# Kernel tuning notes

Hardware: AMD Instinct MI355X
Metric: run time of the kernel (lower is better)

Reference implementation:

```python
import jax, jax.numpy as jnp
import numpy as np

B, DIM, NUM_HEADS = 16384, 2048, 4
SD = DIM // 2            # single_dim = 1024
HD = SD // NUM_HEADS     # head_dim = 256
LH = SD // 4             # lambda-net hidden = 256
SCALE = HD ** -0.5


def setup_inputs() -> dict:
    key = jax.random.key(0)
    ks = jax.random.split(key, 20)
    w = lambda k, shape: jax.random.normal(k, shape, dtype=jnp.float32) * 0.02
    inp = {
        "x": jax.random.normal(ks[0], (B, DIM), dtype=jnp.float32),
        # Linear weights stored (in, out); y = x @ W + b (equivalent to torch Linear)
        "WQ1_w": w(ks[1], (SD, SD)), "WQ1_b": jnp.zeros((SD,), jnp.float32),
        "WK1_w": w(ks[2], (SD, SD)), "WK1_b": jnp.zeros((SD,), jnp.float32),
        "WQ2_w": w(ks[3], (SD, SD)), "WQ2_b": jnp.zeros((SD,), jnp.float32),
        "WK2_w": w(ks[4], (SD, SD)), "WK2_b": jnp.zeros((SD,), jnp.float32),
        "WV_w": w(ks[5], (SD, SD)), "WV_b": jnp.zeros((SD,), jnp.float32),
        "WO_w": w(ks[6], (SD, SD)), "WO_b": jnp.zeros((SD,), jnp.float32),
        "L1_w": w(ks[7], (DIM, LH)), "L1_b": jnp.zeros((LH,), jnp.float32),
        "L2_w": w(ks[8], (LH, 1)), "L2_b": jnp.zeros((1,), jnp.float32),
    }
    return inp


def _heads(t, W, b):
    # tokens [B,2,SD] -> [B,H,2,HD]
    y = t @ W + b
    return y.reshape(B, 2, NUM_HEADS, HD).transpose(0, 2, 1, 3)


def reference(x, WQ1_w, WQ1_b, WK1_w, WK1_b, WQ2_w, WQ2_b, WK2_w, WK2_b,
              WV_w, WV_b, WO_w, WO_b, L1_w, L1_b, L2_w, L2_b):
    tokens = x.reshape(B, 2, SD)
    # gating lambda in (0,1): MLP(x) -> [B,1,1,1]
    lam = jax.nn.sigmoid(jax.nn.relu(x @ L1_w + L1_b) @ L2_w + L2_b)
    lam = lam.reshape(B, 1, 1, 1)

    Q1 = _heads(tokens, WQ1_w, WQ1_b)
    K1 = _heads(tokens, WK1_w, WK1_b)
    Q2 = _heads(tokens, WQ2_w, WQ2_b)
    K2 = _heads(tokens, WK2_w, WK2_b)
    V = _heads(tokens, WV_w, WV_b)

    attn1 = jax.nn.softmax(jnp.einsum("bhqd,bhkd->bhqk", Q1, K1) * SCALE, axis=-1)
    attn2 = jax.nn.softmax(jnp.einsum("bhqd,bhkd->bhqk", Q2, K2) * SCALE, axis=-1)
    diff_attn = jax.nn.relu(attn1 - lam * attn2)  # dropout = identity (eval)

    out = jnp.einsum("bhqk,bhkd->bhqd", diff_attn, V)  # [B,H,2,HD]
    out = out.transpose(0, 2, 1, 3).reshape(B, 2, SD)
    out = (out @ WO_w + WO_b) + tokens
    return out.reshape(B, SD * 2)
```

## Files before the change

### kernel.cpp

```cpp
#include <hip/hip_runtime.h>
#include <stdint.h>


#define BATCH  16384
#define ATT_SCALE 0.0625f

typedef __attribute__((ext_vector_type(8)))  short   s16x8;
typedef __attribute__((ext_vector_type(4)))  float   f32x4;
typedef __attribute__((ext_vector_type(2)))  float   f32x2;
typedef __attribute__((ext_vector_type(8)))  int     i32x8;
typedef __attribute__((ext_vector_type(8)))  unsigned short u16x8;
typedef __attribute__((ext_vector_type(4)))  unsigned short u16x4;

__device__ __forceinline__ unsigned short f2bf(float f) {
  unsigned u = __float_as_uint(f);
  u += 0x7FFFu + ((u >> 16) & 1u);
  return (unsigned short)(u >> 16);
}
__device__ __forceinline__ float bf2f(unsigned short s) {
  return __uint_as_float((unsigned)s << 16);
}

__device__ __forceinline__ unsigned char f2e4m3(float f) {
  unsigned u = __float_as_uint(f);
  unsigned s = (u >> 24) & 0x80u;
  float a = fabsf(f);
  if (a >= 448.f) return (unsigned char)(s | 0x7E);
  if (a < 0.0009765625f) return (unsigned char)s;
  int e = (int)((u >> 23) & 0xFF) - 127;
  if (e < -6) {
    int q = (int)rintf(a * 512.f);
    if (q >= 8) return (unsigned char)(s | 0x08);
    return (unsigned char)(s | q);
  }
  unsigned mant = u & 0x7FFFFFu;
  unsigned mr = mant + 0x7FFFFu + ((mant >> 20) & 1u);
  e += (int)(mr >> 23);
  mant = (mr >> 20) & 7u;
  if (e > 8) return (unsigned char)(s | 0x7E);
  return (unsigned char)(s | ((e + 7) << 3) | mant);
}
__device__ __forceinline__ float e4m3f(unsigned v) {
  unsigned e = (v >> 3) & 15u, m = v & 7u;
  float mag = (e == 0) ? (float)m * 0.001953125f
                       : __uint_as_float(((e + 120u) << 23) | (m << 20));
  return (v & 0x80u) ? -mag : mag;
}

__device__ __forceinline__ unsigned char cvt1_fp8(float v) {
#if __has_builtin(__builtin_amdgcn_cvt_pk_fp8_f32)
  return (unsigned char)(__builtin_amdgcn_cvt_pk_fp8_f32(v, v, 0, false) & 0xff);
#else
  return f2e4m3(v);
#endif
}

__device__ __forceinline__ void dec8(uint2 p, float* o) {
#if __has_builtin(__builtin_amdgcn_cvt_pk_f32_fp8)
  f32x2 a = __builtin_amdgcn_cvt_pk_f32_fp8((int)p.x, false);
  f32x2 b = __builtin_amdgcn_cvt_pk_f32_fp8((int)p.x, true);
  f32x2 c = __builtin_amdgcn_cvt_pk_f32_fp8((int)p.y, false);
  f32x2 d = __builtin_amdgcn_cvt_pk_f32_fp8((int)p.y, true);
  o[0] = a[0]; o[1] = a[1]; o[2] = b[0]; o[3] = b[1];
  o[4] = c[0]; o[5] = c[1]; o[6] = d[0]; o[7] = d[1];
#else
#pragma unroll
  for (int j = 0; j < 4; ++j) o[j]     = e4m3f((p.x >> (8 * j)) & 255u);
#pragma unroll
  for (int j = 0; j < 4; ++j) o[4 + j] = e4m3f((p.y >> (8 * j)) & 255u);
#endif
}

__device__ __forceinline__ void async16(const void* g, void* l) {
  __builtin_amdgcn_global_load_lds((__attribute__((address_space(1))) void*)g,
                                   (__attribute__((address_space(3))) void*)l,
                                   16, 0, 0);
}

__global__ __launch_bounds__(512, 2)
void gemm_mx(const unsigned char* __restrict__ A,
             const unsigned char* __restrict__ Bt,
             const float* __restrict__ bias,
             unsigned char* __restrict__ Cout,
             unsigned char* __restrict__ Vout,
             int NN,
             const unsigned short* __restrict__ xbf,
             const unsigned short* __restrict__ lamBt,
             const float* __restrict__ lamL1b,
             const float* __restrict__ lamL2w,
             float* __restrict__ lamp)
{
  __shared__ __align__(16) char lds[131072];
  const int tid  = threadIdx.x;
  const int lane = tid & 63, w = tid >> 6;
  const int wm = w >> 2, wn = w & 3;
  const int li = lane & 15, lc = lane >> 4;

  if (blockIdx.x < 128) {
    const int bm_l = blockIdx.x * 128;
    const int t = tid;
    const size_t aSrc  = (size_t)(bm_l + (t >> 2)) * 2048 + (t & 3) * 8;
    const size_t b0Src = (size_t)(t >> 2) * 2048 + (t & 3) * 8;
    const size_t b1Src = (size_t)(128 + (t >> 2)) * 2048 + (t & 3) * 8;

    f32x4 acc[4][4];
#pragma unroll
    for (int i = 0; i < 4; ++i)
#pragma unroll
      for (int j = 0; j < 4; ++j) acc[i][j] = (f32x4)0.f;

    for (int k0 = 0; k0 < 2048; k0 += 32) {
      async16(xbf   + aSrc  + k0, lds + w * 1024);
      async16(lamBt + b0Src + k0, lds + 8192 + w * 1024);
      async16(lamBt + b1Src + k0, lds + 16384 + w * 1024);
      __syncthreads();
      s16x8 aR[4], bR[4];
#pragma unroll
      for (int m = 0; m < 4; ++m)
        aR[m] = *(const s16x8*)(lds + ((w >> 2) * 64 + m * 16 + li) * 64 + lc * 16);
#pragma unroll
      for (int n = 0; n < 4; ++n)
        bR[n] = *(const s16x8*)(lds + 8192 + ((w & 3) * 64 + n * 16 + li) * 64 + lc * 16);
#pragma unroll
      for (int m = 0; m < 4; ++m)
#pragma unroll
        for (int n = 0; n < 4; ++n)
          acc[m][n] = __builtin_amdgcn_mfma_f32_16x16x32_bf16(aR[m], bR[n], acc[m][n], 0, 0, 0);
      __syncthreads();
    }

    float l2v[4], bvv[4];
#pragma unroll
    for (int n = 0; n < 4; ++n) {
      const int col = (w & 3) * 64 + n * 16 + li;
      l2v[n] = lamL2w[col];
      bvv[n] = lamL1b[col];
    }
#pragma unroll
    for (int m = 0; m < 4; ++m)
#pragma unroll
      for (int j = 0; j < 4; ++j) {
        float part = 0.f;
#pragma unroll
        for (int n = 0; n < 4; ++n)
          part += fmaxf(acc[m][n][j] + bvv[n], 0.f) * l2v[n];
        part += __shfl_xor(part, 1, 64);
        part += __shfl_xor(part, 2, 64);
        part += __shfl_xor(part, 4, 64);
        part += __shfl_xor(part, 8, 64);
        if ((lane & 15) == 0)
          atomicAdd(lamp + bm_l + (w >> 2) * 64 + m * 16 + lc * 4 + j, part);
      }
    return;
  }

  const int bid = blockIdx.x - 128;
  const int nwg = 2560;
  const int swz = (bid & 7) * (nwg >> 3) + (bid >> 3);
  const int bm = (swz / NN) * 256;
  const int bn = (swz % NN) * 256;

  const int grow   = lane >> 3;
  const int gchunk = ((lane & 7) ^ grow) * 16;
  size_t aSrc[4], bSrc[4];
  int dstKB[4];
#pragma unroll
  for (int i = 0; i < 4; ++i) {
    const int rr = (i * 8 + w) * 8 + grow;
    aSrc[i] = (size_t)(bm + rr) * 1024 + gchunk;
    bSrc[i] = (size_t)(bn + rr) * 1024 + gchunk;
    dstKB[i] = (i * 8 + w) * 1024;
  }

  const int x7   = li & 7;
  const int off0 = ((2 * lc)     ^ x7) * 16;
  const int off1 = ((2 * lc + 1) ^ x7) * 16;
  const int aRow = (wm * 128 + li) * 128;
  const int bRow = 32768 + (wn * 64 + li) * 128;

  f32x4 acc[8][4];
#pragma unroll
  for (int m = 0; m < 8; ++m)
#pragma unroll
    for (int n = 0; n < 4; ++n) acc[m][n] = (f32x4)0.f;

#pragma unroll
  for (int i = 0; i < 4; ++i) {
    async16(A  + aSrc[i], lds + dstKB[i]);
    async16(Bt + bSrc[i], lds + 32768 + dstKB[i]);
  }
#pragma unroll
  for (int i = 0; i < 4; ++i) {
    async16(A  + aSrc[i] + 128, lds + 65536 + dstKB[i]);
    async16(Bt + bSrc[i] + 128, lds + 98304 + dstKB[i]);
  }
  asm volatile("s_waitcnt vmcnt(8)" ::: "memory");
  __builtin_amdgcn_s_barrier();

  for (int t = 0; t < 8; ++t) {
    char* buf = lds + (t & 1) * 65536;

    i32x8 bF[4];
#pragma unroll
    for (int nf = 0; nf < 4; ++nf) {
      const char* p = buf + bRow + nf * 2048;
      uint4* bp = (uint4*)&bF[nf];
      bp[0] = *(const uint4*)(p + off0);
      bp[1] = *(const uint4*)(p + off1);
    }
#pragma unroll
    for (int mh = 0; mh < 2; ++mh) {
      i32x8 aF[4];
#pragma unroll
      for (int mf = 0; mf < 4; ++mf) {
        const char* p = buf + aRow + (mh * 4 + mf) * 2048;
        uint4* ap = (uint4*)&aF[mf];
        ap[0] = *(const uint4*)(p + off0);
        ap[1] = *(const uint4*)(p + off1);
      }
      __builtin_amdgcn_s_setprio(1);
#pragma unroll
      for (int mf = 0; mf < 4; ++mf)
#pragma unroll
        for (int nf = 0; nf < 4; ++nf)
          acc[mh * 4 + mf][nf] = __builtin_amdgcn_mfma_scale_f32_16x16x128_f8f6f4(
              aF[mf], bF[nf], acc[mh * 4 + mf][nf],
              0, 0, 0, 0x7F7F7F7F, 0, 0x7F7F7F7F);
      __builtin_amdgcn_s_setprio(0);
    }
    __builtin_amdgcn_s_barrier();
    if (t + 2 < 8) {
      const size_t kt = (size_t)(t + 2) * 128;
#pragma unroll
      for (int i = 0; i < 4; ++i) {
        async16(A  + aSrc[i] + kt, buf + dstKB[i]);
        async16(Bt + bSrc[i] + kt, buf + 32768 + dstKB[i]);
      }
    }
    if (t < 6) { asm volatile("s_waitcnt vmcnt(8)" ::: "memory"); }
    else       { asm volatile("s_waitcnt vmcnt(0)" ::: "memory"); }
    __builtin_amdgcn_s_barrier();
  }

  float bv[4];
#pragma unroll
  for (int n = 0; n < 4; ++n) bv[n] = bias[bn + wn * 64 + n * 16 + li];

  if (bn < 4096) {
    unsigned char* wl0 = (unsigned char*)(lds + w * 12288);
#pragma unroll
    for (int mp = 0; mp < 4; ++mp) {
      unsigned char* wl = wl0 + (mp & 1) * 2560;
#pragma unroll
      for (int mi = 0; mi < 2; ++mi)
#pragma unroll
        for (int jj = 0; jj < 4; ++jj) {
          unsigned d = 0;
#pragma unroll
          for (int n = 0; n < 4; ++n) {
            float v = acc[mp * 2 + mi][n][jj] + bv[n];
            d |= (unsigned)cvt1_fp8(v) << (8 * n);
          }
          *(unsigned*)(wl + (mi * 16 + lc * 4 + jj) * 80 + li * 4) = d;
        }
      const size_t base = (size_t)((bm + wm * 128 + mp * 32) >> 5) * 131072
                        + (size_t)((bn >> 6) + wn) * 2048;
      uint4 v0 = *(const uint4*)(wl + (lane >> 2) * 80 + (lane & 3) * 16);
      *(uint4*)(Cout + base + lane * 16) = v0;
      uint4 v1 = *(const uint4*)(wl + (16 + (lane >> 2)) * 80 + (lane & 3) * 16);
      *(uint4*)(Cout + base + 1024 + lane * 16) = v1;
    }
  } else {
    unsigned char* wl0 = (unsigned char*)(lds + w * 12288);
    const int cb = bn - 4096;
#pragma unroll
    for (int mp = 0; mp < 4; ++mp) {
      unsigned char* wl = wl0 + (mp & 1) * 2560;
#pragma unroll
      for (int mi = 0; mi < 2; ++mi)
#pragma unroll
        for (int n = 0; n < 4; ++n)
#pragma unroll
          for (int jj = 0; jj < 4; ++jj) {
            float v = acc[mp * 2 + mi][n][jj] + bv[n];
            wl[(mi * 16 + lc * 4 + jj) * 72 + n * 16 + li] = cvt1_fp8(v);
          }
#pragma unroll
      for (int i = 0; i < 4; ++i) {
        const int rr = i * 8 + (lane >> 3);
        uint2 vv = *(const uint2*)(wl + rr * 72 + (lane & 7) * 8);
        const size_t gi = (size_t)(bm + wm * 128 + mp * 32 + rr) * 1024
                        + cb + wn * 64 + (lane & 7) * 8;
        *(uint2*)(Vout + gi) = vv;
      }
    }
  }
}

__global__ __launch_bounds__(512, 2)
void gemm_womx(const unsigned char* __restrict__ A,
               const unsigned char* __restrict__ Bt,
               const float* __restrict__ bias,
               float* __restrict__ Cout,
               const unsigned short* __restrict__ res)
{
  __shared__ __align__(16) char lds[131072];
  const int tid  = threadIdx.x;
  const int lane = tid & 63, w = tid >> 6;
  const int wm = w >> 2, wn = w & 3;
  const int li = lane & 15, lc = lane >> 4;

  const int swz = (blockIdx.x & 7) * 64 + (blockIdx.x >> 3);
  const int bm = (swz >> 2) * 256;
  const int bn = (swz & 3) * 256;

  const int grow   = lane >> 3;
  const int gchunk = ((lane & 7) ^ grow) * 16;
  size_t aSrc[4], bSrc[4];
  int dstKB[4];
#pragma unroll
  for (int i = 0; i < 4; ++i) {
    const int rr = (i * 8 + w) * 8 + grow;
    aSrc[i] = (size_t)(bm + rr) * 1024 + gchunk;
    bSrc[i] = (size_t)(bn + rr) * 1024 + gchunk;
    dstKB[i] = (i * 8 + w) * 1024;
  }

  const int x7   = li & 7;
  const int off0 = ((2 * lc)     ^ x7) * 16;
  const int off1 = ((2 * lc + 1) ^ x7) * 16;
  const int aRow = (wm * 128 + li) * 128;
  const int bRow = 32768 + (wn * 64 + li) * 128;

  f32x4 acc[8][4];
#pragma unroll
  for (int m = 0; m < 8; ++m)
#pragma unroll
    for (int n = 0; n < 4; ++n) acc[m][n] = (f32x4)0.f;

#pragma unroll
  for (int i = 0; i < 4; ++i) {
    async16(A  + aSrc[i], lds + dstKB[i]);
    async16(Bt + bSrc[i], lds + 32768 + dstKB[i]);
  }
#pragma unroll
  for (int i = 0; i < 4; ++i) {
    async16(A  + aSrc[i] + 128, lds + 65536 + dstKB[i]);
    async16(Bt + bSrc[i] + 128, lds + 98304 + dstKB[i]);
  }
  asm volatile("s_waitcnt vmcnt(8)" ::: "memory");
  __builtin_amdgcn_s_barrier();

  for (int t = 0; t < 8; ++t) {
    char* buf = lds + (t & 1) * 65536;

    i32x8 bF[4];
#pragma unroll
    for (int nf = 0; nf < 4; ++nf) {
      const char* p = buf + bRow + nf * 2048;
      uint4* bp = (uint4*)&bF[nf];
      bp[0] = *(const uint4*)(p + off0);
      bp[1] = *(const uint4*)(p + off1);
    }
#pragma unroll
    for (int mh = 0; mh < 2; ++mh) {
      i32x8 aF[4];
#pragma unroll
      for (int mf = 0; mf < 4; ++mf) {
        const char* p = buf + aRow + (mh * 4 + mf) * 2048;
        uint4* ap = (uint4*)&aF[mf];
        ap[0] = *(const uint4*)(p + off0);
        ap[1] = *(const uint4*)(p + off1);
      }
      __builtin_amdgcn_s_setprio(1);
#pragma unroll
      for (int mf = 0; mf < 4; ++mf)
#pragma unroll
        for (int nf = 0; nf < 4; ++nf)
          acc[mh * 4 + mf][nf] = __builtin_amdgcn_mfma_scale_f32_16x16x128_f8f6f4(
              aF[mf], bF[nf], acc[mh * 4 + mf][nf],
              0, 0, 0, 0x7F7F7F7F, 0, 0x7F7F7F7F);
      __builtin_amdgcn_s_setprio(0);
    }
    __builtin_amdgcn_s_barrier();
    if (t + 2 < 8) {
      const size_t kt = (size_t)(t + 2) * 128;
#pragma unroll
      for (int i = 0; i < 4; ++i) {
        async16(A  + aSrc[i] + kt, buf + dstKB[i]);
        async16(Bt + bSrc[i] + kt, buf + 32768 + dstKB[i]);
      }
    }
    if (t < 6) { asm volatile("s_waitcnt vmcnt(8)" ::: "memory"); }
    else       { asm volatile("s_waitcnt vmcnt(0)" ::: "memory"); }
    __builtin_amdgcn_s_barrier();
  }

  float bv[4];
#pragma unroll
  for (int n = 0; n < 4; ++n) bv[n] = bias[bn + wn * 64 + n * 16 + li];

  float* wl0 = (float*)(lds + w * 12288);
#pragma unroll
  for (int m = 0; m < 8; ++m) {
    float* wl = wl0 + (m & 1) * 1088;
#pragma unroll
    for (int n = 0; n < 4; ++n)
#pragma unroll
      for (int jj = 0; jj < 4; ++jj)
        wl[(lc * 4 + jj) * 68 + li + n * 16] = acc[m][n][jj] + bv[n];
#pragma unroll
    for (int i = 0; i < 4; ++i) {
      const int rr = i * 4 + lc;
      f32x4 vv = *(const f32x4*)(wl + rr * 68 + li * 4);
      const size_t gi = (size_t)(bm + wm * 128 + m * 16 + rr) * 1024
                      + bn + wn * 64 + li * 4;
      const u16x4 rv = *(const u16x4*)(res + gi);
      f32x4 ov;
#pragma unroll
      for (int jj = 0; jj < 4; ++jj) ov[jj] = vv[jj] + bf2f(rv[jj]);
      *(f32x4*)(Cout + gi) = ov;
    }
  }
}

__global__ __launch_bounds__(256)
void attn_kernel(const unsigned char* __restrict__ qk8,
                 const unsigned char* __restrict__ vbuf8,
                 const float* __restrict__ lam_pre,
                 const float* __restrict__ L2b,
                 unsigned char* __restrict__ aout8)
{
  const int b = blockIdx.x;
  const int hd = threadIdx.x >> 6;
  const int lane = threadIdx.x & 63;
  const int g = lane >> 5;
  const int l5 = lane & 31;
  const size_t row = (size_t)(2 * b + g);

  const size_t cbase = (row >> 5) * 131072
                     + (size_t)(hd * 4 + (l5 >> 3)) * 2048
                     + (row & 31) * 64 + (l5 & 7) * 8;
  const uint2 p1 = *(const uint2*)(qk8 + cbase);
  const uint2 p2 = *(const uint2*)(qk8 + cbase + 32768);
  const uint2 p3 = *(const uint2*)(qk8 + cbase + 65536);
  const uint2 p4 = *(const uint2*)(qk8 + cbase + 98304);
  const uint2 pv = *(const uint2*)(vbuf8 + row * 1024 + hd * 256 + l5 * 8);

  float q1[8], k1[8], q2[8], k2[8], vf[8];
  dec8(p1, q1); dec8(p2, k1); dec8(p3, q2); dec8(p4, k2);
  dec8(pv, vf);

  float ss1 = 0.f, sc1 = 0.f, ss2 = 0.f, sc2 = 0.f;
#pragma unroll
  for (int j = 0; j < 8; ++j) {
    const float k1o = __shfl_xor(k1[j], 32, 64);
    const float k2o = __shfl_xor(k2[j], 32, 64);
    ss1 += q1[j] * k1[j]; sc1 += q1[j] * k1o;
    ss2 += q2[j] * k2[j]; sc2 += q2[j] * k2o;
  }
#pragma unroll
  for (int m = 16; m >= 1; m >>= 1) {
    ss1 += __shfl_xor(ss1, m, 64); sc1 += __shfl_xor(sc1, m, 64);
    ss2 += __shfl_xor(ss2, m, 64); sc2 += __shfl_xor(sc2, m, 64);
  }

  float e0 = ss1 * ATT_SCALE, e1 = sc1 * ATT_SCALE;
  float mx = fmaxf(e0, e1);
  float xs = expf(e0 - mx), xc = expf(e1 - mx);
  float inv = 1.f / (xs + xc);
  const float a1s = xs * inv, a1c = xc * inv;

  e0 = ss2 * ATT_SCALE; e1 = sc2 * ATT_SCALE;
  mx = fmaxf(e0, e1);
  xs = expf(e0 - mx); xc = expf(e1 - mx);
  inv = 1.f / (xs + xc);
  const float a2s = xs * inv, a2c = xc * inv;

  const float lm = 1.f / (1.f + expf(-(lam_pre[b] + L2b[0])));
  const float ps = fmaxf(a1s - lm * a2s, 0.f);
  const float pc = fmaxf(a1c - lm * a2c, 0.f);

  unsigned lo = 0, hi = 0;
#pragma unroll
  for (int j = 0; j < 4; ++j) {
    const float vo = __shfl_xor(vf[j], 32, 64);
    lo |= (unsigned)cvt1_fp8(ps * vf[j] + pc * vo) << (8 * j);
  }
#pragma unroll
  for (int j = 4; j < 8; ++j) {
    const float vo = __shfl_xor(vf[j], 32, 64);
    hi |= (unsigned)cvt1_fp8(ps * vf[j] + pc * vo) << (8 * (j - 4));
  }
  uint2 o2; o2.x = lo; o2.y = hi;
  *(uint2*)(aout8 + row * 1024 + hd * 256 + l5 * 8) = o2;
}

__global__ void prep_k(const float* __restrict__ s0, const float* __restrict__ s1,
                       const float* __restrict__ s2, const float* __restrict__ s3,
                       const float* __restrict__ s4, const float* __restrict__ s5,
                       const float* __restrict__ L1w,
                       const float* __restrict__ b0, const float* __restrict__ b1,
                       const float* __restrict__ b2, const float* __restrict__ b3,
                       const float* __restrict__ b4,
                       const float* __restrict__ x,
                       unsigned char* __restrict__ qw8,
                       unsigned char* __restrict__ wot8,
                       unsigned short* __restrict__ l1t,
                       float* __restrict__ bcat,
                       unsigned short* __restrict__ x_bf,
                       unsigned char* __restrict__ x_f8,
                       float* __restrict__ lamp)
{
  __shared__ float tile[32][33];
  const int z = blockIdx.z;
  const int tx = threadIdx.x, ty = threadIdx.y;

  if (z < 6) {
    const float* W;
    switch (z) {
      case 0: W = s0; break;
      case 1: W = s1; break;
      case 2: W = s2; break;
      case 3: W = s3; break;
      case 4: W = s4; break;
      default: W = s5; break;
    }
    const int bn = blockIdx.x * 32, bk = blockIdx.y * 32;
#pragma unroll
    for (int i = ty; i < 32; i += 8)
      tile[i][tx] = W[(size_t)(bk + i) * 1024 + bn + tx];
    __syncthreads();
    unsigned char* Wt = (z < 5) ? (qw8 + (size_t)z * 1048576) : wot8;
#pragma unroll
    for (int i = ty; i < 32; i += 8)
      Wt[(size_t)(bn + i) * 1024 + bk + tx] = cvt1_fp8(tile[tx][i]);
    return;
  }
  if (z < 22) {
    const int c = (z - 6) * 1024 + blockIdx.y * 32 + blockIdx.x;
    const int i = c * 256 + ty * 32 + tx;
    const float4* p = (const float4*)x + (size_t)i * 2;
    float4 a = p[0], b = p[1];
    float f[8] = {a.x, a.y, a.z, a.w, b.x, b.y, b.z, b.w};
    u16x8 v; unsigned lo = 0, hi = 0;
#pragma unroll
    for (int j = 0; j < 8; ++j) v[j] = f2bf(f[j]);
#pragma unroll
    for (int j = 0; j < 4; ++j) lo |= (unsigned)cvt1_fp8(f[j]) << (8 * j);
#pragma unroll
    for (int j = 0; j < 4; ++j) hi |= (unsigned)cvt1_fp8(f[4 + j]) << (8 * j);
    *(u16x8*)(x_bf + (size_t)i * 8) = v;
    uint2 c8; c8.x = lo; c8.y = hi;
    *(uint2*)(x_f8 + (size_t)i * 8) = c8;
    return;
  }
  if (z == 22) {
    const int idx = blockIdx.y * 32 + blockIdx.x;
    if (idx >= 512) return;
    const int bn = (idx & 7) * 32, bk = (idx >> 3) * 32;
#pragma unroll
    for (int i = ty; i < 32; i += 8)
      tile[i][tx] = L1w[(size_t)(bk + i) * 256 + bn + tx];
    __syncthreads();
#pragma unroll
    for (int i = ty; i < 32; i += 8)
      l1t[(size_t)(bn + i) * 2048 + bk + tx] = f2bf(tile[tx][i]);
    return;
  }
  const int idx = blockIdx.y * 32 + blockIdx.x;
  const int t = ty * 32 + tx;
  if (idx < 20) {
    const int i = idx * 256 + t;
    const float* src;
    switch (i >> 10) {
      case 0: src = b0; break;
      case 1: src = b1; break;
      case 2: src = b2; break;
      case 3: src = b3; break;
      default: src = b4; break;
    }
    bcat[i] = src[i & 1023];
  } else if (idx < 84) {
    lamp[(idx - 20) * 256 + t] = 0.f;
  }
}

extern "C" void kernel_launch(void* const* d_in, const int* in_sizes, int n_in,
                              void* d_out, int out_size, void* d_ws, size_t ws_size,
                              hipStream_t stream)
{
  const float* x    = (const float*)d_in[0];
  const float* WQ1w = (const float*)d_in[1];  const float* WQ1b = (const float*)d_in[2];
  const float* WK1w = (const float*)d_in[3];  const float* WK1b = (const float*)d_in[4];
  const float* WQ2w = (const float*)d_in[5];  const float* WQ2b = (const float*)d_in[6];
  const float* WK2w = (const float*)d_in[7];  const float* WK2b = (const float*)d_in[8];
  const float* WVw  = (const float*)d_in[9];  const float* WVb  = (const float*)d_in[10];
  const float* WOw  = (const float*)d_in[11]; const float* WOb  = (const float*)d_in[12];
  const float* L1w  = (const float*)d_in[13]; const float* L1b  = (const float*)d_in[14];
  const float* L2w  = (const float*)d_in[15]; const float* L2b  = (const float*)d_in[16];

  char* ws = (char*)d_ws;
  size_t off = 0;
  unsigned short* x_bf  = (unsigned short*)(ws + off); off += (size_t)33554432 * 2;
  unsigned char*  x_f8  = (unsigned char*)(ws + off);  off += (size_t)33554432;
  unsigned char*  qw8   = (unsigned char*)(ws + off);  off += (size_t)5242880;
  unsigned char*  wot8  = (unsigned char*)(ws + off);  off += (size_t)1048576;
  unsigned short* l1t   = (unsigned short*)(ws + off); off += (size_t)524288 * 2;
  float*          bcat  = (float*)(ws + off);          off += (size_t)5120 * 4;
  unsigned char*  qk8   = (unsigned char*)(ws + off);  off += (size_t)32768 * 4096;
  unsigned char*  vbuf8 = (unsigned char*)(ws + off);  off += (size_t)33554432;
  unsigned char*  abuf8 = (unsigned char*)(ws + off);  off += (size_t)33554432;
  float*          lamp  = (float*)(ws + off);          off += (size_t)16384 * 4;

  prep_k<<<dim3(32, 32, 24), dim3(32, 8), 0, stream>>>(
      WQ1w, WK1w, WQ2w, WK2w, WVw, WOw, L1w,
      WQ1b, WK1b, WQ2b, WK2b, WVb, x,
      qw8, wot8, l1t, bcat, x_bf, x_f8, lamp);

  gemm_mx<<<dim3(128 + 2560), 512, 0, stream>>>(
      x_f8, qw8, bcat, qk8, vbuf8, 20, x_bf, l1t, L1b, L2w, lamp);

  attn_kernel<<<16384, 256, 0, stream>>>(qk8, vbuf8, lamp, L2b, abuf8);

  gemm_womx<<<dim3(512), 512, 0, stream>>>(
      abuf8, wot8, WOb, (float*)d_out, x_bf);
}
```

Before: 396.4 us.

## Shrink GEMM tiles to 128x128 with 256-thread blocks and single-buffered LDS

```diff
diff --git a/kernel.cpp b/kernel.cpp
--- a/kernel.cpp
+++ b/kernel.cpp
@@ -2,7 +2,6 @@
 #include <stdint.h>
 
 
-#define BATCH  16384
 #define ATT_SCALE 0.0625f
 
 typedef __attribute__((ext_vector_type(8)))  short   s16x8;
@@ -77,31 +76,29 @@
                                    16, 0, 0);
 }
 
-__global__ __launch_bounds__(512, 2)
+__global__ __launch_bounds__(256, 4)
 void gemm_mx(const unsigned char* __restrict__ A,
              const unsigned char* __restrict__ Bt,
              const float* __restrict__ bias,
              unsigned char* __restrict__ Cout,
              unsigned char* __restrict__ Vout,
-             int NN,
              const unsigned short* __restrict__ xbf,
              const unsigned short* __restrict__ lamBt,
              const float* __restrict__ lamL1b,
              const float* __restrict__ lamL2w,
              float* __restrict__ lamp)
 {
-  __shared__ __align__(16) char lds[131072];
+  __shared__ __align__(16) char lds[32768];
   const int tid  = threadIdx.x;
   const int lane = tid & 63, w = tid >> 6;
-  const int wm = w >> 2, wn = w & 3;
   const int li = lane & 15, lc = lane >> 4;
 
-  if (blockIdx.x < 128) {
-    const int bm_l = blockIdx.x * 128;
-    const int t = tid;
-    const size_t aSrc  = (size_t)(bm_l + (t >> 2)) * 2048 + (t & 3) * 8;
-    const size_t b0Src = (size_t)(t >> 2) * 2048 + (t & 3) * 8;
-    const size_t b1Src = (size_t)(128 + (t >> 2)) * 2048 + (t & 3) * 8;
+  if (blockIdx.x < 256) {
+    unsigned short* lA = (unsigned short*)lds;
+    unsigned short* lB = (unsigned short*)(lds + 8192);
+    const int wm = w >> 1, wn = w & 1;
+    const int bm = (blockIdx.x >> 1) * 128;
+    const int bn = (blockIdx.x & 1) * 128;
 
     f32x4 acc[4][4];
 #pragma unroll
@@ -109,33 +106,43 @@
 #pragma unroll
       for (int j = 0; j < 4; ++j) acc[i][j] = (f32x4)0.f;
 
+    const int ar = tid >> 2;
+    const int ac = (tid & 3) * 8;
+    const unsigned short* aG0 = xbf   + (size_t)(bm + ar) * 2048 + ac;
+    const unsigned short* aG1 = aG0 + (size_t)64 * 2048;
+    const unsigned short* bG0 = lamBt + (size_t)(bn + ar) * 2048 + ac;
+    const unsigned short* bG1 = bG0 + (size_t)64 * 2048;
+    unsigned short* aL0 = lA + w * 512;
+    unsigned short* aL1 = lA + 2048 + w * 512;
+    unsigned short* bL0 = lB + w * 512;
+    unsigned short* bL1 = lB + 2048 + w * 512;
+
+    const unsigned short* aF = lA + (wm * 64 + li) * 32 + lc * 8;
+    const unsigned short* bF = lB + (wn * 64 + li) * 32 + lc * 8;
+
     for (int k0 = 0; k0 < 2048; k0 += 32) {
-      async16(xbf   + aSrc  + k0, lds + w * 1024);
-      async16(lamBt + b0Src + k0, lds + 8192 + w * 1024);
-      async16(lamBt + b1Src + k0, lds + 16384 + w * 1024);
+      async16(aG0, aL0); async16(aG1, aL1);
+      async16(bG0, bL0); async16(bG1, bL1);
+      aG0 += 32; aG1 += 32; bG0 += 32; bG1 += 32;
       __syncthreads();
-      s16x8 aR[4], bR[4];
+      s16x8 af[4], bw[4];
+#pragma unroll
+      for (int m = 0; m < 4; ++m) af[m] = *(const s16x8*)(aF + m * 512);
+#pragma unroll
+      for (int n = 0; n < 4; ++n) bw[n] = *(const s16x8*)(bF + n * 512);
 #pragma unroll
       for (int m = 0; m < 4; ++m)
-        aR[m] = *(const s16x8*)(lds + ((w >> 2) * 64 + m * 16 + li) * 64 + lc * 16);
-#pragma unroll
-      for (int n = 0; n < 4; ++n)
-        bR[n] = *(const s16x8*)(lds + 8192 + ((w & 3) * 64 + n * 16 + li) * 64 + lc * 16);
-#pragma unroll
-      for (int m = 0; m < 4; ++m)
 #pragma unroll
         for (int n = 0; n < 4; ++n)
-          acc[m][n] = __builtin_amdgcn_mfma_f32_16x16x32_bf16(aR[m], bR[n], acc[m][n], 0, 0, 0);
+          acc[m][n] = __builtin_amdgcn_mfma_f32_16x16x32_bf16(af[m], bw[n], acc[m][n], 0, 0, 0);
       __syncthreads();
     }
 
+    const int r0 = bm + wm * 64 + (lc << 2);
+    const int c0 = bn + wn * 64 + li;
     float l2v[4], bvv[4];
 #pragma unroll
-    for (int n = 0; n < 4; ++n) {
-      const int col = (w & 3) * 64 + n * 16 + li;
-      l2v[n] = lamL2w[col];
-      bvv[n] = lamL1b[col];
-    }
+    for (int n = 0; n < 4; ++n) { l2v[n] = lamL2w[c0 + n * 16]; bvv[n] = lamL1b[c0 + n * 16]; }
 #pragma unroll
     for (int m = 0; m < 4; ++m)
 #pragma unroll
@@ -148,273 +155,240 @@
         part += __shfl_xor(part, 2, 64);
         part += __shfl_xor(part, 4, 64);
         part += __shfl_xor(part, 8, 64);
-        if ((lane & 15) == 0)
-          atomicAdd(lamp + bm_l + (w >> 2) * 64 + m * 16 + lc * 4 + j, part);
+        if ((lane & 15) == 0) atomicAdd(lamp + r0 + m * 16 + j, part);
       }
     return;
   }
 
-  const int bid = blockIdx.x - 128;
-  const int nwg = 2560;
-  const int swz = (bid & 7) * (nwg >> 3) + (bid >> 3);
-  const int bm = (swz / NN) * 256;
-  const int bn = (swz % NN) * 256;
-
-  const int grow   = lane >> 3;
-  const int gchunk = ((lane & 7) ^ grow) * 16;
-  size_t aSrc[4], bSrc[4];
-  int dstKB[4];
+  const int bid = blockIdx.x - 256;
+  const int swz = (bid & 7) * 1280 + (bid >> 3);
+  const int bm = (swz / 40) * 128;
+  const int bn = (swz % 40) * 128;
+  const int wr = w >> 1, wc = w & 1;
+
+  const int srow   = tid >> 3;
+  const int schunk = ((tid & 7) ^ (srow & 7)) * 16;
+  size_t aS[4], bS[4];
+  int dA[4], dB[4];
 #pragma unroll
   for (int i = 0; i < 4; ++i) {
-    const int rr = (i * 8 + w) * 8 + grow;
-    aSrc[i] = (size_t)(bm + rr) * 1024 + gchunk;
-    bSrc[i] = (size_t)(bn + rr) * 1024 + gchunk;
-    dstKB[i] = (i * 8 + w) * 1024;
+    aS[i] = (size_t)(bm + i * 32 + srow) * 1024 + schunk;
+    bS[i] = (size_t)(bn + i * 32 + srow) * 1024 + schunk;
+    dA[i] = i * 4096 + srow * 128 + (tid & 7) * 16;
+    dB[i] = 16384 + dA[i];
   }
 
   const int x7   = li & 7;
   const int off0 = ((2 * lc)     ^ x7) * 16;
   const int off1 = ((2 * lc + 1) ^ x7) * 16;
-  const int aRow = (wm * 128 + li) * 128;
-  const int bRow = 32768 + (wn * 64 + li) * 128;
-
-  f32x4 acc[8][4];
-#pragma unroll
-  for (int m = 0; m < 8; ++m)
+  const int aBase = (wr * 64 + li) * 128;
+  const int bBase = 16384 + (wc * 64 + li) * 128;
+
+  f32x4 acc[4][4];
+#pragma unroll
+  for (int m = 0; m < 4; ++m)
 #pragma unroll
     for (int n = 0; n < 4; ++n) acc[m][n] = (f32x4)0.f;
 
 #pragma unroll
   for (int i = 0; i < 4; ++i) {
-    async16(A  + aSrc[i], lds + dstKB[i]);
-    async16(Bt + bSrc[i], lds + 32768 + dstKB[i]);
-  }
-#pragma unroll
-  for (int i = 0; i < 4; ++i) {
-    async16(A  + aSrc[i] + 128, lds + 65536 + dstKB[i]);
-    async16(Bt + bSrc[i] + 128, lds + 98304 + dstKB[i]);
-  }
-  asm volatile("s_waitcnt vmcnt(8)" ::: "memory");
-  __builtin_amdgcn_s_barrier();
+    async16(A  + aS[i], lds + dA[i]);
+    async16(Bt + bS[i], lds + dB[i]);
+  }
 
   for (int t = 0; t < 8; ++t) {
-    char* buf = lds + (t & 1) * 65536;
+    asm volatile("s_waitcnt vmcnt(0)" ::: "memory");
+    __builtin_amdgcn_s_barrier();
 
     i32x8 bF[4];
 #pragma unroll
     for (int nf = 0; nf < 4; ++nf) {
-      const char* p = buf + bRow + nf * 2048;
+      const char* p = lds + bBase + nf * 2048;
       uint4* bp = (uint4*)&bF[nf];
       bp[0] = *(const uint4*)(p + off0);
       bp[1] = *(const uint4*)(p + off1);
     }
-#pragma unroll
-    for (int mh = 0; mh < 2; ++mh) {
-      i32x8 aF[4];
-#pragma unroll
-      for (int mf = 0; mf < 4; ++mf) {
-        const char* p = buf + aRow + (mh * 4 + mf) * 2048;
-        uint4* ap = (uint4*)&aF[mf];
-        ap[0] = *(const uint4*)(p + off0);
-        ap[1] = *(const uint4*)(p + off1);
+    __builtin_amdgcn_s_setprio(1);
+#pragma unroll
+    for (int mf = 0; mf < 4; ++mf) {
+      i32x8 aF;
+      const char* p = lds + aBase + mf * 2048;
+      uint4* ap = (uint4*)&aF;
+      ap[0] = *(const uint4*)(p + off0);
+      ap[1] = *(const uint4*)(p + off1);
+#pragma unroll
+      for (int nf = 0; nf < 4; ++nf)
+        acc[mf][nf] = __builtin_amdgcn_mfma_scale_f32_16x16x128_f8f6f4(
+            aF, bF[nf], acc[mf][nf], 0, 0, 0, 0x7F7F7F7F, 0, 0x7F7F7F7F);
+    }
+    __builtin_amdgcn_s_setprio(0);
+    __builtin_amdgcn_s_barrier();
+    if (t < 7) {
+      const size_t kt = (size_t)(t + 1) * 128;
+#pragma unroll
+      for (int i = 0; i < 4; ++i) {
+        async16(A  + aS[i] + kt, lds + dA[i]);
+        async16(Bt + bS[i] + kt, lds + dB[i]);
       }
-      __builtin_amdgcn_s_setprio(1);
-#pragma unroll
-      for (int mf = 0; mf < 4; ++mf)
-#pragma unroll
-        for (int nf = 0; nf < 4; ++nf)
-          acc[mh * 4 + mf][nf] = __builtin_amdgcn_mfma_scale_f32_16x16x128_f8f6f4(
-              aF[mf], bF[nf], acc[mh * 4 + mf][nf],
-              0, 0, 0, 0x7F7F7F7F, 0, 0x7F7F7F7F);
-      __builtin_amdgcn_s_setprio(0);
-    }
-    __builtin_amdgcn_s_barrier();
-    if (t + 2 < 8) {
-      const size_t kt = (size_t)(t + 2) * 128;
-#pragma unroll
-      for (int i = 0; i < 4; ++i) {
-        async16(A  + aSrc[i] + kt, buf + dstKB[i]);
-        async16(Bt + bSrc[i] + kt, buf + 32768 + dstKB[i]);
+    }
+  }
+
+  float bv[4];
+#pragma unroll
+  for (int n = 0; n < 4; ++n) bv[n] = bias[bn + wc * 64 + n * 16 + li];
+
+  char* wl = lds + w * 8192;
+  if (bn < 4096) {
+#pragma unroll
+    for (int m = 0; m < 4; ++m)
+#pragma unroll
+      for (int jj = 0; jj < 4; ++jj) {
+        unsigned d = 0;
+#pragma unroll
+        for (int n = 0; n < 4; ++n) {
+          float v = acc[m][n][jj] + bv[n];
+          d |= (unsigned)cvt1_fp8(v) << (8 * n);
+        }
+        *(unsigned*)(wl + (m * 16 + lc * 4 + jj) * 72 + li * 4) = d;
       }
-    }
-    if (t < 6) { asm volatile("s_waitcnt vmcnt(8)" ::: "memory"); }
-    else       { asm volatile("s_waitcnt vmcnt(0)" ::: "memory"); }
-    __builtin_amdgcn_s_barrier();
-  }
-
-  float bv[4];
-#pragma unroll
-  for (int n = 0; n < 4; ++n) bv[n] = bias[bn + wn * 64 + n * 16 + li];
-
-  if (bn < 4096) {
-    unsigned char* wl0 = (unsigned char*)(lds + w * 12288);
-#pragma unroll
-    for (int mp = 0; mp < 4; ++mp) {
-      unsigned char* wl = wl0 + (mp & 1) * 2560;
-#pragma unroll
-      for (int mi = 0; mi < 2; ++mi)
+    const int R0 = bm + wr * 64;
+    const int C0 = bn + wc * 64;
+#pragma unroll
+    for (int h = 0; h < 2; ++h) {
+      const size_t base = (size_t)((R0 + h * 32) >> 5) * 131072
+                        + (size_t)(C0 >> 6) * 2048;
+      const int row = lane >> 1, off = (lane & 1) * 32;
+      uint4 v0 = *(const uint4*)(wl + (h * 32 + row) * 72 + off);
+      uint4 v1 = *(const uint4*)(wl + (h * 32 + row) * 72 + off + 16);
+      *(uint4*)(Cout + base + lane * 32)      = v0;
+      *(uint4*)(Cout + base + lane * 32 + 16) = v1;
+    }
+  } else {
+    const int cb = bn - 4096 + wc * 64;
+#pragma unroll
+    for (int m = 0; m < 4; ++m)
+#pragma unroll
+      for (int n = 0; n < 4; ++n)
 #pragma unroll
         for (int jj = 0; jj < 4; ++jj) {
-          unsigned d = 0;
-#pragma unroll
-          for (int n = 0; n < 4; ++n) {
-            float v = acc[mp * 2 + mi][n][jj] + bv[n];
-            d |= (unsigned)cvt1_fp8(v) << (8 * n);
-          }
-          *(unsigned*)(wl + (mi * 16 + lc * 4 + jj) * 80 + li * 4) = d;
+          float v = acc[m][n][jj] + bv[n];
+          wl[(m * 16 + lc * 4 + jj) * 72 + n * 16 + li] = cvt1_fp8(v);
         }
-      const size_t base = (size_t)((bm + wm * 128 + mp * 32) >> 5) * 131072
-                        + (size_t)((bn >> 6) + wn) * 2048;
-      uint4 v0 = *(const uint4*)(wl + (lane >> 2) * 80 + (lane & 3) * 16);
-      *(uint4*)(Cout + base + lane * 16) = v0;
-      uint4 v1 = *(const uint4*)(wl + (16 + (lane >> 2)) * 80 + (lane & 3) * 16);
-      *(uint4*)(Cout + base + 1024 + lane * 16) = v1;
-    }
-  } else {
-    unsigned char* wl0 = (unsigned char*)(lds + w * 12288);
-    const int cb = bn - 4096;
-#pragma unroll
-    for (int mp = 0; mp < 4; ++mp) {
-      unsigned char* wl = wl0 + (mp & 1) * 2560;
-#pragma unroll
-      for (int mi = 0; mi < 2; ++mi)
-#pragma unroll
-        for (int n = 0; n < 4; ++n)
-#pragma unroll
-          for (int jj = 0; jj < 4; ++jj) {
-            float v = acc[mp * 2 + mi][n][jj] + bv[n];
-            wl[(mi * 16 + lc * 4 + jj) * 72 + n * 16 + li] = cvt1_fp8(v);
-          }
-#pragma unroll
-      for (int i = 0; i < 4; ++i) {
-        const int rr = i * 8 + (lane >> 3);
-        uint2 vv = *(const uint2*)(wl + rr * 72 + (lane & 7) * 8);
-        const size_t gi = (size_t)(bm + wm * 128 + mp * 32 + rr) * 1024
-                        + cb + wn * 64 + (lane & 7) * 8;
-        *(uint2*)(Vout + gi) = vv;
-      }
-    }
-  }
-}
-
-__global__ __launch_bounds__(512, 2)
+    const int R0 = bm + wr * 64;
+    const int row = lane >> 1, off = (lane & 1) * 32;
+    uint4 v0 = *(const uint4*)(wl + row * 72 + off);
+    uint4 v1 = *(const uint4*)(wl + row * 72 + off + 16);
+    uint4 v2 = *(const uint4*)(wl + (32 + row) * 72 + off);
+    uint4 v3 = *(const uint4*)(wl + (32 + row) * 72 + off + 16);
+    *(uint4*)(Vout + (size_t)(R0 + row) * 1024 + cb + off)           = v0;
+    *(uint4*)(Vout + (size_t)(R0 + row) * 1024 + cb + off + 16)      = v1;
+    *(uint4*)(Vout + (size_t)(R0 + 32 + row) * 1024 + cb + off)      = v2;
+    *(uint4*)(Vout + (size_t)(R0 + 32 + row) * 1024 + cb + off + 16) = v3;
+  }
+}
+
+__global__ __launch_bounds__(256, 4)
 void gemm_womx(const unsigned char* __restrict__ A,
                const unsigned char* __restrict__ Bt,
                const float* __restrict__ bias,
                float* __restrict__ Cout,
                const unsigned short* __restrict__ res)
 {
-  __shared__ __align__(16) char lds[131072];
+  __shared__ __align__(16) char lds[32768];
   const int tid  = threadIdx.x;
   const int lane = tid & 63, w = tid >> 6;
-  const int wm = w >> 2, wn = w & 3;
   const int li = lane & 15, lc = lane >> 4;
-
-  const int swz = (blockIdx.x & 7) * 64 + (blockIdx.x >> 3);
-  const int bm = (swz >> 2) * 256;
-  const int bn = (swz & 3) * 256;
-
-  const int grow   = lane >> 3;
-  const int gchunk = ((lane & 7) ^ grow) * 16;
-  size_t aSrc[4], bSrc[4];
-  int dstKB[4];
+  const int wr = w >> 1, wc = w & 1;
+
+  const int swz = (blockIdx.x & 7) * 256 + (blockIdx.x >> 3);
+  const int bm = (swz >> 3) * 128;
+  const int bn = (swz & 7) * 128;
+
+  const int srow   = tid >> 3;
+  const int schunk = ((tid & 7) ^ (srow & 7)) * 16;
+  size_t aS[4], bS[4];
+  int dA[4], dB[4];
 #pragma unroll
   for (int i = 0; i < 4; ++i) {
-    const int rr = (i * 8 + w) * 8 + grow;
-    aSrc[i] = (size_t)(bm + rr) * 1024 + gchunk;
-    bSrc[i] = (size_t)(bn + rr) * 1024 + gchunk;
-    dstKB[i] = (i * 8 + w) * 1024;
+    aS[i] = (size_t)(bm + i * 32 + srow) * 1024 + schunk;
+    bS[i] = (size_t)(bn + i * 32 + srow) * 1024 + schunk;
+    dA[i] = i * 4096 + srow * 128 + (tid & 7) * 16;
+    dB[i] = 16384 + dA[i];
   }
 
   const int x7   = li & 7;
   const int off0 = ((2 * lc)     ^ x7) * 16;
   const int off1 = ((2 * lc + 1) ^ x7) * 16;
-  const int aRow = (wm * 128 + li) * 128;
-  const int bRow = 32768 + (wn * 64 + li) * 128;
-
-  f32x4 acc[8][4];
-#pragma unroll
-  for (int m = 0; m < 8; ++m)
+  const int aBase = (wr * 64 + li) * 128;
+  const int bBase = 16384 + (wc * 64 + li) * 128;
+
+  f32x4 acc[4][4];
+#pragma unroll
+  for (int m = 0; m < 4; ++m)
 #pragma unroll
     for (int n = 0; n < 4; ++n) acc[m][n] = (f32x4)0.f;
 
 #pragma unroll
   for (int i = 0; i < 4; ++i) {
-    async16(A  + aSrc[i], lds + dstKB[i]);
-    async16(Bt + bSrc[i], lds + 32768 + dstKB[i]);
-  }
-#pragma unroll
-  for (int i = 0; i < 4; ++i) {
-    async16(A  + aSrc[i] + 128, lds + 65536 + dstKB[i]);
-    async16(Bt + bSrc[i] + 128, lds + 98304 + dstKB[i]);
-  }
-  asm volatile("s_waitcnt vmcnt(8)" ::: "memory");
-  __builtin_amdgcn_s_barrier();
+    async16(A  + aS[i], lds + dA[i]);
+    async16(Bt + bS[i], lds + dB[i]);
+  }
 
   for (int t = 0; t < 8; ++t) {
-    char* buf = lds + (t & 1) * 65536;
+    asm volatile("s_waitcnt vmcnt(0)" ::: "memory");
+    __builtin_amdgcn_s_barrier();
 
     i32x8 bF[4];
 #pragma unroll
     for (int nf = 0; nf < 4; ++nf) {
-      const char* p = buf + bRow + nf * 2048;
+      const char* p = lds + bBase + nf * 2048;
       uint4* bp = (uint4*)&bF[nf];
       bp[0] = *(const uint4*)(p + off0);
       bp[1] = *(const uint4*)(p + off1);
     }
-#pragma unroll
-    for (int mh = 0; mh < 2; ++mh) {
-      i32x8 aF[4];
-#pragma unroll
-      for (int mf = 0; mf < 4; ++mf) {
-        const char* p = buf + aRow + (mh * 4 + mf) * 2048;
-        uint4* ap = (uint4*)&aF[mf];
-        ap[0] = *(const uint4*)(p + off0);
-        ap[1] = *(const uint4*)(p + off1);
+    __builtin_amdgcn_s_setprio(1);
+#pragma unroll
+    for (int mf = 0; mf < 4; ++mf) {
+      i32x8 aF;
+      const char* p = lds + aBase + mf * 2048;
+      uint4* ap = (uint4*)&aF;
+      ap[0] = *(const uint4*)(p + off0);
+      ap[1] = *(const uint4*)(p + off1);
+#pragma unroll
+      for (int nf = 0; nf < 4; ++nf)
+        acc[mf][nf] = __builtin_amdgcn_mfma_scale_f32_16x16x128_f8f6f4(
+            aF, bF[nf], acc[mf][nf], 0, 0, 0, 0x7F7F7F7F, 0, 0x7F7F7F7F);
+    }
+    __builtin_amdgcn_s_setprio(0);
+    __builtin_amdgcn_s_barrier();
+    if (t < 7) {
+      const size_t kt = (size_t)(t + 1) * 128;
+#pragma unroll
+      for (int i = 0; i < 4; ++i) {
+        async16(A  + aS[i] + kt, lds + dA[i]);
+        async16(Bt + bS[i] + kt, lds + dB[i]);
       }
-      __builtin_amdgcn_s_setprio(1);
-#pragma unroll
-      for (int mf = 0; mf < 4; ++mf)
-#pragma unroll
-        for (int nf = 0; nf < 4; ++nf)
-          acc[mh * 4 + mf][nf] = __builtin_amdgcn_mfma_scale_f32_16x16x128_f8f6f4(
-              aF[mf], bF[nf], acc[mh * 4 + mf][nf],
-              0, 0, 0, 0x7F7F7F7F, 0, 0x7F7F7F7F);
-      __builtin_amdgcn_s_setprio(0);
-    }
-    __builtin_amdgcn_s_barrier();
-    if (t + 2 < 8) {
-      const size_t kt = (size_t)(t + 2) * 128;
-#pragma unroll
-      for (int i = 0; i < 4; ++i) {
-        async16(A  + aSrc[i] + kt, buf + dstKB[i]);
-        async16(Bt + bSrc[i] + kt, buf + 32768 + dstKB[i]);
-      }
-    }
-    if (t < 6) { asm volatile("s_waitcnt vmcnt(8)" ::: "memory"); }
-    else       { asm volatile("s_waitcnt vmcnt(0)" ::: "memory"); }
-    __builtin_amdgcn_s_barrier();
+    }
   }
 
   float bv[4];
 #pragma unroll
-  for (int n = 0; n < 4; ++n) bv[n] = bias[bn + wn * 64 + n * 16 + li];
-
-  float* wl0 = (float*)(lds + w * 12288);
-#pragma unroll
-  for (int m = 0; m < 8; ++m) {
-    float* wl = wl0 + (m & 1) * 1088;
+  for (int n = 0; n < 4; ++n) bv[n] = bias[bn + wc * 64 + n * 16 + li];
+
+  float* wl = (float*)(lds + w * 8192);
+#pragma unroll
+  for (int m = 0; m < 4; ++m) {
 #pragma unroll
     for (int n = 0; n < 4; ++n)
 #pragma unroll
       for (int jj = 0; jj < 4; ++jj)
-        wl[(lc * 4 + jj) * 68 + li + n * 16] = acc[m][n][jj] + bv[n];
+        wl[(lc * 4 + jj) * 68 + n * 16 + li] = acc[m][n][jj] + bv[n];
 #pragma unroll
     for (int i = 0; i < 4; ++i) {
       const int rr = i * 4 + lc;
       f32x4 vv = *(const f32x4*)(wl + rr * 68 + li * 4);
-      const size_t gi = (size_t)(bm + wm * 128 + m * 16 + rr) * 1024
-                      + bn + wn * 64 + li * 4;
+      const size_t gi = (size_t)(bm + wr * 64 + m * 16 + rr) * 1024
+                      + bn + wc * 64 + li * 4;
       const u16x4 rv = *(const u16x4*)(res + gi);
       f32x4 ov;
 #pragma unroll
@@ -618,11 +592,11 @@
       WQ1b, WK1b, WQ2b, WK2b, WVb, x,
       qw8, wot8, l1t, bcat, x_bf, x_f8, lamp);
 
-  gemm_mx<<<dim3(128 + 2560), 512, 0, stream>>>(
-      x_f8, qw8, bcat, qk8, vbuf8, 20, x_bf, l1t, L1b, L2w, lamp);
+  gemm_mx<<<dim3(256 + 10240), 256, 0, stream>>>(
+      x_f8, qw8, bcat, qk8, vbuf8, x_bf, l1t, L1b, L2w, lamp);
 
   attn_kernel<<<16384, 256, 0, stream>>>(qk8, vbuf8, lamp, L2b, abuf8);
 
-  gemm_womx<<<dim3(512), 512, 0, stream>>>(
+  gemm_womx<<<dim3(2048), 256, 0, stream>>>(
       abuf8, wot8, WOb, (float*)d_out, x_bf);
 }
```

After: 589.3 us. 48.7% more time.
